# Performance work log

Measured on AMD Instinct MI355X. Metric: run time of the kernel, lower is better.

Reference implementation:

```python
import jax, jax.numpy as jnp
import numpy as np

B, S, H = 2, 2048, 2048
NH, HD = 16, 128


def rotate_half(x):
    x1, x2 = x[..., : x.shape[-1] // 2], x[..., x.shape[-1] // 2 :]
    return jnp.concatenate((-x2, x1), axis=-1)


def setup_inputs() -> dict:
    key = jax.random.key(0)
    ks = jax.random.split(key, 8)
    return {
        "hidden": jax.random.normal(ks[0], (B, S, H), dtype=jnp.float32),
        "cos": jax.random.uniform(ks[1], (S, HD), dtype=jnp.float32),
        "sin": jax.random.uniform(ks[2], (S, HD), dtype=jnp.float32),
        "attention_mask": jnp.zeros((B, 1, S, S), dtype=jnp.float32),
        "Wq": jax.random.normal(ks[3], (H, H), dtype=jnp.float32) * 0.02,
        "Wk": jax.random.normal(ks[4], (H, H), dtype=jnp.float32) * 0.02,
        "Wv": jax.random.normal(ks[5], (H, H), dtype=jnp.float32) * 0.02,
        "Wo": jax.random.normal(ks[6], (H, H), dtype=jnp.float32) * 0.02,
    }


def reference(hidden, cos, sin, attention_mask, Wq, Wk, Wv, Wo):
    b, s, h = hidden.shape
    # torch Linear: y = x @ W.T ; reshape to [B, NH, S, HD]
    def proj(W):
        return (hidden @ W.T).reshape(b, s, NH, HD).transpose(0, 2, 1, 3)

    q, k, v = proj(Wq), proj(Wk), proj(Wv)
    c = cos[None, None, :, :]  # [1,1,S,HD]
    si = sin[None, None, :, :]
    q = q * c + rotate_half(q) * si
    k = k * c + rotate_half(k) * si
    scores = jnp.einsum("bhqd,bhkd->bhqk", q, k) / jnp.sqrt(jnp.float32(HD))
    scores = scores + attention_mask
    attn = jax.nn.softmax(scores.astype(jnp.float32), axis=-1).astype(q.dtype)
    out = jnp.einsum("bhqk,bhkd->bhqd", attn, v)
    out = out.transpose(0, 2, 1, 3).reshape(b, s, h)
    return out @ Wo.T
```

## Files before the change

kernel.cpp:

```cpp
#include <hip/hip_runtime.h>
#include <hip/hip_bf16.h>
#include <math.h>

#define SEQ 2048
#define HID 2048
#define NHEAD 16
#define HDIM 128
#define LDK 4096

typedef __bf16 bf16_t;
typedef __bf16 bf16x2 __attribute__((ext_vector_type(2)));
typedef __bf16 bf16x4_t __attribute__((ext_vector_type(4)));
typedef __bf16 bf16x8 __attribute__((ext_vector_type(8)));
typedef float f32x4 __attribute__((ext_vector_type(4)));
typedef float f32x16 __attribute__((ext_vector_type(16)));
typedef unsigned u32x4 __attribute__((ext_vector_type(4)));

#define MFMA16(a, b, c) __builtin_amdgcn_mfma_f32_16x16x32_bf16(a, b, c, 0, 0, 0)
#define MFMA32(a, b, c) __builtin_amdgcn_mfma_f32_32x32x16_bf16(a, b, c, 0, 0, 0)
#define GLOAD_LDS(g, l) \
  __builtin_amdgcn_global_load_lds((const __attribute__((address_space(1))) void*)(g), \
                                   (__attribute__((address_space(3))) void*)(l), 16, 0, 0)

static __device__ inline unsigned pk2(float lo, float hi) {
  bf16x2 t; t[0] = (bf16_t)lo; t[1] = (bf16_t)hi;
  return __builtin_bit_cast(unsigned, t);
}

static __device__ inline bf16x8 pack_slice(const float* p, int hi) {
  unsigned A1 = pk2(p[0], p[1]);
  unsigned A2 = pk2(p[2], p[3]);
  unsigned B1 = pk2(p[4], p[5]);
  unsigned B2 = pk2(p[6], p[7]);
  unsigned A1s = __shfl_xor(A1, 32, 64);
  unsigned A2s = __shfl_xor(A2, 32, 64);
  unsigned B1s = __shfl_xor(B1, 32, 64);
  unsigned B2s = __shfl_xor(B2, 32, 64);
  unsigned w0 = hi ? B1s : A1;
  unsigned w1 = hi ? B2s : A2;
  unsigned w2 = hi ? B1 : A1s;
  unsigned w3 = hi ? B2 : A2s;
  u32x4 W = {w0, w1, w2, w3};
  return __builtin_bit_cast(bf16x8, W);
}

__global__ void cast_hidden(const float* __restrict__ in, bf16_t* __restrict__ out) {
  int i = blockIdx.x * 256 + threadIdx.x;
  float4 v = ((const float4*)in)[i];
  bf16x4_t b;
  b[0] = (bf16_t)v.x; b[1] = (bf16_t)v.y; b[2] = (bf16_t)v.z; b[3] = (bf16_t)v.w;
  ((bf16x4_t*)out)[i] = b;
}

__global__ void cast_weights(const float* __restrict__ a, const float* __restrict__ b,
                             const float* __restrict__ c, const float* __restrict__ d,
                             bf16_t* __restrict__ out) {
  const float* srcs[4] = {a, b, c, d};
  const float* src = srcs[blockIdx.y];
  bf16_t* dst = out + (size_t)blockIdx.y * (HID * HID);
  int i = blockIdx.x * 256 + threadIdx.x;
  float4 v = ((const float4*)src)[i];
  bf16x4_t o;
  o[0] = (bf16_t)v.x; o[1] = (bf16_t)v.y; o[2] = (bf16_t)v.z; o[3] = (bf16_t)v.w;
  ((bf16x4_t*)dst)[i] = o;
}

__global__ __launch_bounds__(512, 2) void gemm256(
    const bf16_t* __restrict__ A, const bf16_t* __restrict__ Bw,
    bf16_t* __restrict__ Cb, float* __restrict__ Cf, int M, int N, int K) {
  __shared__ char smem[131072];
  const int tid = threadIdx.x, lane = tid & 63, wid = tid >> 6;
  const int wr = wid >> 2, wc = wid & 3;
  const int lr = lane & 15, lg = lane >> 4;
  const int xcd = blockIdx.x & 7, l = blockIdx.x >> 3;
  const int brow = (xcd >> 2) * 8 + (l >> 2);
  const int bcol = (xcd & 3) * 4 + (l & 3);
  const int NT = K >> 6;

  const bf16_t* Ab = A + (size_t)(brow * 256) * K;
  const bf16_t* Bb = Bw + (size_t)(bcol * 256) * K;

  f32x4 acc[8][4] = {};
  bf16x8 af[4], bfr[4];
  const int swz = (lg ^ ((lr >> 1) & 3)) << 4;

#define STAGE_HALF(t_, op, kh)                                                        \
  {                                                                                   \
    int tt = (t_) < NT ? (t_) : NT - 1;                                               \
    const bf16_t* gsrc = (op) ? Bb : Ab;                                              \
    char* ldst = smem + (tt & 1) * 65536 + (op) * 32768 + (kh) * 16384;               \
    _Pragma("unroll") for (int is = 0; is < 2; ++is) {                                \
      int p = tid + is * 512;                                                         \
      int row = p >> 2, ch = p & 3;                                                   \
      GLOAD_LDS(gsrc + (size_t)row * K + tt * 64 + (kh) * 32 +                        \
                    ((ch ^ ((row >> 1) & 3)) * 8),                                    \
                ldst + p * 16);                                                       \
    }                                                                                 \
  }

#define PHASE(cb, kh, mh, LOADB, STAGECALL, VM)                                       \
  {                                                                                   \
    _Pragma("unroll") for (int mf = 0; mf < 4; ++mf) {                                \
      int row = wr * 128 + (mh) * 64 + mf * 16 + lr;                                  \
      af[mf] = *(const bf16x8*)(smem + (cb) * 65536 + (kh) * 16384 + row * 64 + swz); \
    }                                                                                 \
    if (LOADB) {                                                                      \
      _Pragma("unroll") for (int nf = 0; nf < 4; ++nf) {                              \
        int row = wc * 64 + nf * 16 + lr;                                             \
        bfr[nf] = *(const bf16x8*)(smem + (cb) * 65536 + 32768 + (kh) * 16384 +       \
                                   row * 64 + swz);                                   \
      }                                                                               \
    }                                                                                 \
    STAGECALL;                                                                        \
    __builtin_amdgcn_s_barrier();                                                     \
    asm volatile("s_waitcnt lgkmcnt(0)" ::: "memory");                                \
    __builtin_amdgcn_sched_barrier(0);                                                \
    __builtin_amdgcn_s_setprio(1);                                                    \
    _Pragma("unroll") for (int mf = 0; mf < 4; ++mf)                                  \
      _Pragma("unroll") for (int nf = 0; nf < 4; ++nf)                                \
        acc[(mh) * 4 + mf][nf] = MFMA16(af[mf], bfr[nf], acc[(mh) * 4 + mf][nf]);     \
    __builtin_amdgcn_s_setprio(0);                                                    \
    if (VM) { asm volatile("s_waitcnt vmcnt(6)" ::: "memory"); }                      \
    __builtin_amdgcn_s_barrier();                                                     \
    __builtin_amdgcn_sched_barrier(0);                                                \
  }

  STAGE_HALF(0, 1, 0); STAGE_HALF(0, 0, 0); STAGE_HALF(0, 1, 1); STAGE_HALF(0, 0, 1);
  STAGE_HALF(1, 1, 0); STAGE_HALF(1, 0, 0); STAGE_HALF(1, 1, 1);
  asm volatile("s_waitcnt vmcnt(6)" ::: "memory");
  __builtin_amdgcn_s_barrier();
  __builtin_amdgcn_sched_barrier(0);

  const int NI = NT >> 1;
  for (int i = 0; i < NI; ++i) {
    const int t2 = 2 * i;
    PHASE(0, 0, 0, 1, STAGE_HALF(t2 + 1, 0, 1), 0);
    PHASE(0, 0, 1, 0, STAGE_HALF(t2 + 2, 1, 0), 0);
    PHASE(0, 1, 0, 1, STAGE_HALF(t2 + 2, 0, 0), 0);
    PHASE(0, 1, 1, 0, STAGE_HALF(t2 + 2, 1, 1), 1);
    PHASE(1, 0, 0, 1, STAGE_HALF(t2 + 2, 0, 1), 0);
    PHASE(1, 0, 1, 0, STAGE_HALF(t2 + 3, 1, 0), 0);
    PHASE(1, 1, 0, 1, STAGE_HALF(t2 + 3, 0, 0), 0);
    PHASE(1, 1, 1, 0, STAGE_HALF(t2 + 3, 1, 1), 1);
  }
#undef PHASE
#undef STAGE_HALF

#pragma unroll
  for (int mi = 0; mi < 8; ++mi)
#pragma unroll
    for (int nf = 0; nf < 4; ++nf)
#pragma unroll
      for (int r = 0; r < 4; ++r) {
        int row = brow * 256 + wr * 128 + (mi >> 2) * 64 + (mi & 3) * 16 + lg * 4 + r;
        int col = bcol * 256 + wc * 64 + nf * 16 + lr;
        float v = acc[mi][nf][r];
        if (Cf) Cf[(size_t)row * N + col] = v;
        else    Cb[(size_t)row * N + col] = (bf16_t)v;
      }
}

__global__ __launch_bounds__(256, 3) void gemm_bt(
    const bf16_t* __restrict__ A, const bf16_t* __restrict__ Bw,
    bf16_t* __restrict__ Cb, float* __restrict__ Cf,
    int M, int N, int K) {
  __shared__ bf16_t As[2][128 * 32];
  __shared__ bf16_t Bs[2][128 * 32];
  const int tid = threadIdx.x;
  const int lane = tid & 63, wid = tid >> 6;
  const int wr = wid >> 1, wc = wid & 1;
  const int lr = lane & 15, lg = lane >> 4;
  const int nwg = gridDim.x;
  const int lid = (blockIdx.x & 7) * (nwg >> 3) + (blockIdx.x >> 3);
  const int nbc = N >> 7;
  const int brow = lid / nbc, bcol = lid % nbc;

  f32x4 acc[4][4] = {};
  const int swz = lg ^ ((lr >> 1) & 3);

  const int srow = tid >> 2, sch = tid & 3;
#define GSTAGE(k0, bb)                                                                   \
  {                                                                                      \
    _Pragma("unroll") for (int is = 0; is < 2; ++is) {                                   \
      int row = srow + is * 64;                                                          \
      int g = (sch ^ ((row >> 1) & 3)) * 8;                                              \
      GLOAD_LDS(A + (size_t)(brow * 128 + row) * K + (k0) + g,                           \
                &As[bb][(row * 4 + sch) * 8]);                                           \
      GLOAD_LDS(Bw + (size_t)(bcol * 128 + row) * K + (k0) + g,                          \
                &Bs[bb][(row * 4 + sch) * 8]);                                           \
    }                                                                                    \
  }

  GSTAGE(0, 0);
  __syncthreads();

  const int nt = K / 32;
  for (int t = 0; t < nt; ++t) {
    const int cb = t & 1;
    if (t + 1 < nt) GSTAGE((t + 1) * 32, cb ^ 1);
    bf16x8 af[4], bfr[4];
#pragma unroll
    for (int m = 0; m < 4; ++m)
      af[m] = *(const bf16x8*)(&As[cb][(wr * 64 + m * 16 + lr) * 32 + swz * 8]);
#pragma unroll
    for (int n = 0; n < 4; ++n)
      bfr[n] = *(const bf16x8*)(&Bs[cb][(wc * 64 + n * 16 + lr) * 32 + swz * 8]);
#pragma unroll
    for (int m = 0; m < 4; ++m)
#pragma unroll
      for (int n = 0; n < 4; ++n)
        acc[m][n] = MFMA16(af[m], bfr[n], acc[m][n]);
    __syncthreads();
  }
#undef GSTAGE

#pragma unroll
  for (int m = 0; m < 4; ++m)
#pragma unroll
    for (int n = 0; n < 4; ++n)
#pragma unroll
      for (int r = 0; r < 4; ++r) {
        int row = brow * 128 + wr * 64 + m * 16 + lg * 4 + r;
        int col = bcol * 128 + wc * 64 + n * 16 + lr;
        float v = acc[m][n][r];
        if (Cf) Cf[(size_t)row * N + col] = v;
        else    Cb[(size_t)row * N + col] = (bf16_t)v;
      }
}

__global__ void rope_qk(bf16_t* __restrict__ QK,
                        const float* __restrict__ cost, const float* __restrict__ sint) {
  const float SCALE = 0.08838834764831845f;
  int idx = blockIdx.x * 256 + threadIdx.x;
  int d8 = idx & 7;
  int t = idx >> 3;
  int h = t & 15;
  int row = t >> 4;
  int s = row & (SEQ - 1);
  size_t base = (size_t)row * LDK + h * HDIM;
  const float4* cp = (const float4*)(cost + s * HDIM);
  const float4* sp = (const float4*)(sint + s * HDIM);
  float4 c0a = cp[d8 * 2], c0b = cp[d8 * 2 + 1];
  float4 c1a = cp[16 + d8 * 2], c1b = cp[16 + d8 * 2 + 1];
  float4 s0a = sp[d8 * 2], s0b = sp[d8 * 2 + 1];
  float4 s1a = sp[16 + d8 * 2], s1b = sp[16 + d8 * 2 + 1];
  float c0[8] = {c0a.x, c0a.y, c0a.z, c0a.w, c0b.x, c0b.y, c0b.z, c0b.w};
  float c1[8] = {c1a.x, c1a.y, c1a.z, c1a.w, c1b.x, c1b.y, c1b.z, c1b.w};
  float s0[8] = {s0a.x, s0a.y, s0a.z, s0a.w, s0b.x, s0b.y, s0b.z, s0b.w};
  float s1[8] = {s1a.x, s1a.y, s1a.z, s1a.w, s1b.x, s1b.y, s1b.z, s1b.w};

  bf16_t* Q = QK;
  bf16_t* K = QK + 2048;
  bf16x8 qlo = *(bf16x8*)(Q + base + d8 * 8);
  bf16x8 qhi = *(bf16x8*)(Q + base + 64 + d8 * 8);
  bf16x8 klo = *(bf16x8*)(K + base + d8 * 8);
  bf16x8 khi = *(bf16x8*)(K + base + 64 + d8 * 8);
  bf16x8 qlo2, qhi2, klo2, khi2;
#pragma unroll
  for (int j = 0; j < 8; ++j) {
    float q0 = (float)qlo[j], q1 = (float)qhi[j];
    qlo2[j] = (bf16_t)((q0 * c0[j] - q1 * s0[j]) * SCALE);
    qhi2[j] = (bf16_t)((q1 * c1[j] + q0 * s1[j]) * SCALE);
    float k0 = (float)klo[j], k1 = (float)khi[j];
    klo2[j] = (bf16_t)(k0 * c0[j] - k1 * s0[j]);
    khi2[j] = (bf16_t)(k1 * c1[j] + k0 * s1[j]);
  }
  *(bf16x8*)(Q + base + d8 * 8) = qlo2;
  *(bf16x8*)(Q + base + 64 + d8 * 8) = qhi2;
  *(bf16x8*)(K + base + d8 * 8) = klo2;
  *(bf16x8*)(K + base + 64 + d8 * 8) = khi2;
}

__global__ void transpose_v(const bf16_t* __restrict__ Vf, bf16_t* __restrict__ Vt) {
  __shared__ bf16_t t[32][33];
  int tx = threadIdx.x & 31, ty = threadIdx.x >> 5;
  int r0 = blockIdx.y * 32, c0 = blockIdx.x * 32;
#pragma unroll
  for (int j = 0; j < 4; ++j)
    t[ty + j * 8][tx] = Vf[(size_t)(r0 + ty + j * 8) * HID + c0 + tx];
  __syncthreads();
#pragma unroll
  for (int j = 0; j < 4; ++j) {
    int c = c0 + ty + j * 8;
    int r = r0 + tx;
    int h = c >> 7, d = c & 127, b = r >> 11, s = r & (SEQ - 1);
    Vt[(((size_t)(b * NHEAD + h)) * HDIM + d) * SEQ + s] = t[tx][ty + j * 8];
  }
}

__global__ void mask_pack(const float* __restrict__ m, bf16_t* __restrict__ mp) {
  __shared__ float t[32][33];
  int tx = threadIdx.x & 31, ty = threadIdx.x >> 5;
  int q0 = blockIdx.x * 32, k0 = blockIdx.y * 32;
  const float* mb = m + (size_t)blockIdx.z * SEQ * SEQ;
#pragma unroll
  for (int j = 0; j < 4; ++j)
    t[ty + j * 8][tx] = mb[(size_t)(q0 + ty + j * 8) * SEQ + k0 + tx];
  __syncthreads();
  int r = tx & 15, hi = tx >> 4;
  int kl = (r & 3) + 8 * (r >> 2) + 4 * hi;
  bf16_t* ob = mp + ((size_t)(blockIdx.z * 64 + blockIdx.y) * 2048 + q0) * 32;
#pragma unroll
  for (int j = 0; j < 4; ++j) {
    int qloc = ty + j * 8;
    ob[(size_t)qloc * 32 + tx] = (bf16_t)t[qloc][kl];
  }
}

__global__ __launch_bounds__(512, 2) void flash_fwd(
    const bf16_t* __restrict__ Qf, const bf16_t* __restrict__ Kf,
    const bf16_t* __restrict__ Vt, const bf16_t* __restrict__ maskP,
    bf16_t* __restrict__ AO) {
  __shared__ char smem[131072];
  char* KsB = smem;
  char* VsB = smem + 65536;
  const int tid = threadIdx.x, lane = tid & 63, wid = tid >> 6;
  const int q32 = lane & 31, hi = lane >> 5;

  const int x = blockIdx.x;
  const int bh = x & 31, qt = x >> 5;
  const int b = bh >> 4, h = bh & 15;
  const int qg = qt * 256 + wid * 32 + q32;

  bf16x8 qf[8];
  const bf16_t* qptr = Qf + (size_t)(b * SEQ + qg) * LDK + h * HDIM + hi * 8;
#pragma unroll
  for (int ds = 0; ds < 8; ++ds) qf[ds] = *(const bf16x8*)(qptr + ds * 16);

  const bf16_t* mQ = maskP + (size_t)b * 64 * 65536 + (size_t)qg * 32 + hi * 16;

  float mrun = -INFINITY, lpart = 0.f;
  f32x16 o[4] = {};
  const int lswz = (q32 & 15) << 4;

#define STAGE_KV(kt_, bb)                                                                \
  {                                                                                      \
    const int kb0_ = (kt_) * 128;                                                        \
    _Pragma("unroll") for (int is = 0; is < 4; ++is) {                                   \
      int p = tid + is * 512;                                                            \
      int row = p >> 4, ch = p & 15;                                                     \
      int src = (ch * 16) ^ ((row & 15) << 4);                                           \
      GLOAD_LDS((const char*)(Kf + (size_t)(b * SEQ + kb0_ + row) * LDK + h * HDIM) +    \
                    src,                                                                 \
                KsB + (bb) * 32768 + p * 16);                                            \
      GLOAD_LDS((const char*)(Vt + (size_t)(bh * HDIM + row) * SEQ + kb0_) + src,        \
                VsB + (bb) * 32768 + p * 16);                                            \
    }                                                                                    \
  }

  STAGE_KV(0, 0);
  __syncthreads();

  const int NT = SEQ / 128;
  for (int kt = 0; kt < NT; ++kt) {
    const int cur = kt & 1;
    if (kt + 1 < NT) STAGE_KV(kt + 1, cur ^ 1);

    bf16x8 mk[8];
#pragma unroll
    for (int kb = 0; kb < 4; ++kb) {
      const size_t mo = (size_t)(kt * 4 + kb) * 65536;
      mk[2 * kb]     = *(const bf16x8*)(mQ + mo);
      mk[2 * kb + 1] = *(const bf16x8*)(mQ + mo + 8);
    }
    f32x16 sacc[4];
#pragma unroll
    for (int kb = 0; kb < 4; ++kb)
#pragma unroll
      for (int r = 0; r < 8; ++r) {
        sacc[kb][r]     = (float)mk[2 * kb][r];
        sacc[kb][8 + r] = (float)mk[2 * kb + 1][r];
      }

    const char* Kbase = KsB + cur * 32768 + q32 * 256;
#pragma unroll
    for (int ds = 0; ds < 8; ++ds) {
      const int co = (ds * 32 + hi * 16) ^ lswz;
#pragma unroll
      for (int kb = 0; kb < 4; ++kb) {
        bf16x8 kfr = *(const bf16x8*)(Kbase + kb * 8192 + co);
        sacc[kb] = MFMA32(kfr, qf[ds], sacc[kb]);
      }
    }

    f32x16 mm;
#pragma unroll
    for (int r = 0; r < 16; ++r)
      mm[r] = fmaxf(fmaxf(sacc[0][r], sacc[1][r]), fmaxf(sacc[2][r], sacc[3][r]));
    float e0 = fmaxf(fmaxf(mm[0], mm[1]), fmaxf(mm[2], mm[3]));
    float e1 = fmaxf(fmaxf(mm[4], mm[5]), fmaxf(mm[6], mm[7]));
    float e2 = fmaxf(fmaxf(mm[8], mm[9]), fmaxf(mm[10], mm[11]));
    float e3 = fmaxf(fmaxf(mm[12], mm[13]), fmaxf(mm[14], mm[15]));
    float mx = fmaxf(fmaxf(e0, e1), fmaxf(e2, e3));
    mx = fmaxf(mx, __shfl_xor(mx, 32, 64));
    if (!__all(mx <= mrun + 8.f)) {
      float mnew = fmaxf(mrun, mx);
      float corr = __expf(mrun - mnew);
      mrun = mnew; lpart *= corr;
#pragma unroll
      for (int d0 = 0; d0 < 4; ++d0)
#pragma unroll
        for (int r = 0; r < 16; ++r) o[d0][r] *= corr;
    }

#pragma unroll
    for (int kb = 0; kb < 4; ++kb) {
      float p_[16];
#pragma unroll
      for (int r = 0; r < 16; ++r) p_[r] = __expf(sacc[kb][r] - mrun);
      {
        float t0 = (p_[0] + p_[1]) + (p_[2] + p_[3]);
        float t1 = (p_[4] + p_[5]) + (p_[6] + p_[7]);
        float t2 = (p_[8] + p_[9]) + (p_[10] + p_[11]);
        float t3 = (p_[12] + p_[13]) + (p_[14] + p_[15]);
        lpart += (t0 + t1) + (t2 + t3);
      }
#pragma unroll
      for (int s = 0; s < 2; ++s) {
        bf16x8 pav = pack_slice(p_ + 8 * s, hi);
        const int gs = kb * 2 + s;
        const char* Vbase = VsB + cur * 32768 + q32 * 256;
#pragma unroll
        for (int d0 = 0; d0 < 4; ++d0) {
          bf16x8 vf = *(const bf16x8*)(Vbase + d0 * 8192 +
                                       ((gs * 32 + hi * 16) ^ lswz));
          o[d0] = MFMA32(vf, pav, o[d0]);
        }
      }
    }
    __syncthreads();
  }
#undef STAGE_KV

  float l = lpart + __shfl_xor(lpart, 32, 64);
  float rl = 1.f / l;
  bf16_t* aorow = AO + (size_t)(b * SEQ + qg) * HID + h * HDIM;
#pragma unroll
  for (int d0 = 0; d0 < 4; ++d0)
#pragma unroll
    for (int g = 0; g < 4; ++g) {
      unsigned lo = pk2(o[d0][4 * g + 0] * rl, o[d0][4 * g + 1] * rl);
      unsigned hi2 = pk2(o[d0][4 * g + 2] * rl, o[d0][4 * g + 3] * rl);
      int d = d0 * 32 + 8 * g + 4 * hi;
      *(unsigned*)(aorow + d) = lo;
      *(unsigned*)(aorow + d + 2) = hi2;
    }
}

extern "C" void kernel_launch(void* const* d_in, const int* in_sizes, int n_in,
                              void* d_out, int out_size, void* d_ws, size_t ws_size,
                              hipStream_t stream) {
  const float* hidden = (const float*)d_in[0];
  const float* cost   = (const float*)d_in[1];
  const float* sint   = (const float*)d_in[2];
  const float* mask   = (const float*)d_in[3];
  const float* Wq     = (const float*)d_in[4];
  const float* Wk     = (const float*)d_in[5];
  const float* Wv     = (const float*)d_in[6];
  const float* Wo     = (const float*)d_in[7];
  float* out = (float*)d_out;
  char* ws = (char*)d_ws;

  bf16_t* Af    = (bf16_t*)(ws + 0);
  bf16_t* Wqb   = (bf16_t*)(ws + 16777216);
  bf16_t* Wvb   = (bf16_t*)(ws + 33554432);
  bf16_t* Wob   = (bf16_t*)(ws + 41943040);
  bf16_t* QK    = (bf16_t*)(ws + 50331648);
  bf16_t* Vf    = (bf16_t*)(ws + 83886080);
  bf16_t* Vt    = (bf16_t*)(ws + 0);
  bf16_t* maskP = (bf16_t*)(ws + 83886080);
  bf16_t* AO    = (bf16_t*)(ws + 16777216);

  cast_hidden<<<8192, 256, 0, stream>>>(hidden, Af);
  cast_weights<<<dim3(4096, 4), 256, 0, stream>>>(Wq, Wk, Wv, Wo, Wqb);

  gemm256<<<256, 512, 0, stream>>>(Af, Wqb, QK, nullptr, 4096, LDK, HID);
  gemm_bt<<<512, 256, 0, stream>>>(Af, Wvb, Vf, nullptr, 4096, HID, HID);

  rope_qk<<<2048, 256, 0, stream>>>(QK, cost, sint);
  transpose_v<<<dim3(64, 128), 256, 0, stream>>>(Vf, Vt);
  mask_pack<<<dim3(64, 64, 2), 256, 0, stream>>>(mask, maskP);

  flash_fwd<<<256, 512, 0, stream>>>(QK, QK + 2048, Vt, maskP, AO);

  gemm_bt<<<512, 256, 0, stream>>>(AO, Wob, nullptr, out, 4096, HID, HID);
}
```

Baseline: 319.8 us.

## Pipeline QK MFMA chains with per-block softmax using exp2 and permlane swap

Restructures the flash attention inner loop so the QK^T chain for key block kb+1 is issued before the softmax and PV work for block kb, keeping a per-block online max instead of one max per 128-key tile. Folds log2(e) into the Q scale and the packed mask so the softmax can use raw v_exp_f32 (exp2) rather than __expf. Replaces four shuffles plus selects in P packing with v_permlane32_swap. Adds s_setprio around MFMA chains and raises the lazy-rescale threshold to suit base-2. Checking the max more often may trigger more rescales, and the interleaving adds register pressure.

```diff
diff --git a/kernel.cpp b/kernel.cpp
--- a/kernel.cpp
+++ b/kernel.cpp
@@ -27,20 +27,20 @@
   return __builtin_bit_cast(unsigned, t);
 }
 
-static __device__ inline bf16x8 pack_slice(const float* p, int hi) {
+static __device__ inline float exp2_fast(float x) {
+  float r;
+  asm("v_exp_f32 %0, %1" : "=v"(r) : "v"(x));
+  return r;
+}
+
+static __device__ inline bf16x8 pack_slice(const float* p) {
   unsigned A1 = pk2(p[0], p[1]);
   unsigned A2 = pk2(p[2], p[3]);
   unsigned B1 = pk2(p[4], p[5]);
   unsigned B2 = pk2(p[6], p[7]);
-  unsigned A1s = __shfl_xor(A1, 32, 64);
-  unsigned A2s = __shfl_xor(A2, 32, 64);
-  unsigned B1s = __shfl_xor(B1, 32, 64);
-  unsigned B2s = __shfl_xor(B2, 32, 64);
-  unsigned w0 = hi ? B1s : A1;
-  unsigned w1 = hi ? B2s : A2;
-  unsigned w2 = hi ? B1 : A1s;
-  unsigned w3 = hi ? B2 : A2s;
-  u32x4 W = {w0, w1, w2, w3};
+  asm("v_permlane32_swap_b32 %0, %1" : "+v"(A1), "+v"(B1));
+  asm("v_permlane32_swap_b32 %0, %1" : "+v"(A2), "+v"(B2));
+  u32x4 W = {A1, A2, B1, B2};
   return __builtin_bit_cast(bf16x8, W);
 }
 
@@ -230,7 +230,7 @@
 
 __global__ void rope_qk(bf16_t* __restrict__ QK,
                         const float* __restrict__ cost, const float* __restrict__ sint) {
-  const float SCALE = 0.08838834764831845f;
+  const float SCALE = 0.12751569978848444f;
   int idx = blockIdx.x * 256 + threadIdx.x;
   int d8 = idx & 7;
   int t = idx >> 3;
@@ -289,6 +289,7 @@
 }
 
 __global__ void mask_pack(const float* __restrict__ m, bf16_t* __restrict__ mp) {
+  const float L2E = 1.4426950408889634f;
   __shared__ float t[32][33];
   int tx = threadIdx.x & 31, ty = threadIdx.x >> 5;
   int q0 = blockIdx.x * 32, k0 = blockIdx.y * 32;
@@ -303,7 +304,7 @@
 #pragma unroll
   for (int j = 0; j < 4; ++j) {
     int qloc = ty + j * 8;
-    ob[(size_t)qloc * 32 + tx] = (bf16_t)t[qloc][kl];
+    ob[(size_t)qloc * 32 + tx] = (bf16_t)(t[qloc][kl] * L2E);
   }
 }
 
@@ -348,6 +349,24 @@
     }                                                                                    \
   }
 
+#define INIT_SACC(kb)                                                                    \
+  {                                                                                      \
+    _Pragma("unroll") for (int r = 0; r < 8; ++r) {                                      \
+      sacc[kb][r]     = (float)mk[2 * (kb)][r];                                          \
+      sacc[kb][8 + r] = (float)mk[2 * (kb) + 1][r];                                      \
+    }                                                                                    \
+  }
+#define QK_CHAIN(kb)                                                                     \
+  {                                                                                      \
+    const char* Kb_ = KsB + cur * 32768 + q32 * 256 + (kb) * 8192;                       \
+    __builtin_amdgcn_s_setprio(1);                                                       \
+    _Pragma("unroll") for (int ds = 0; ds < 8; ++ds) {                                   \
+      bf16x8 kfr = *(const bf16x8*)(Kb_ + ((ds * 32 + hi * 16) ^ lswz));                 \
+      sacc[kb] = MFMA32(kfr, qf[ds], sacc[kb]);                                          \
+    }                                                                                    \
+    __builtin_amdgcn_s_setprio(0);                                                       \
+  }
+
   STAGE_KV(0, 0);
   __syncthreads();
 
@@ -363,51 +382,38 @@
       mk[2 * kb]     = *(const bf16x8*)(mQ + mo);
       mk[2 * kb + 1] = *(const bf16x8*)(mQ + mo + 8);
     }
+
     f32x16 sacc[4];
-#pragma unroll
-    for (int kb = 0; kb < 4; ++kb)
-#pragma unroll
-      for (int r = 0; r < 8; ++r) {
-        sacc[kb][r]     = (float)mk[2 * kb][r];
-        sacc[kb][8 + r] = (float)mk[2 * kb + 1][r];
-      }
-
-    const char* Kbase = KsB + cur * 32768 + q32 * 256;
-#pragma unroll
-    for (int ds = 0; ds < 8; ++ds) {
-      const int co = (ds * 32 + hi * 16) ^ lswz;
-#pragma unroll
-      for (int kb = 0; kb < 4; ++kb) {
-        bf16x8 kfr = *(const bf16x8*)(Kbase + kb * 8192 + co);
-        sacc[kb] = MFMA32(kfr, qf[ds], sacc[kb]);
-      }
-    }
-
-    f32x16 mm;
-#pragma unroll
-    for (int r = 0; r < 16; ++r)
-      mm[r] = fmaxf(fmaxf(sacc[0][r], sacc[1][r]), fmaxf(sacc[2][r], sacc[3][r]));
-    float e0 = fmaxf(fmaxf(mm[0], mm[1]), fmaxf(mm[2], mm[3]));
-    float e1 = fmaxf(fmaxf(mm[4], mm[5]), fmaxf(mm[6], mm[7]));
-    float e2 = fmaxf(fmaxf(mm[8], mm[9]), fmaxf(mm[10], mm[11]));
-    float e3 = fmaxf(fmaxf(mm[12], mm[13]), fmaxf(mm[14], mm[15]));
-    float mx = fmaxf(fmaxf(e0, e1), fmaxf(e2, e3));
-    mx = fmaxf(mx, __shfl_xor(mx, 32, 64));
-    if (!__all(mx <= mrun + 8.f)) {
-      float mnew = fmaxf(mrun, mx);
-      float corr = __expf(mrun - mnew);
-      mrun = mnew; lpart *= corr;
-#pragma unroll
-      for (int d0 = 0; d0 < 4; ++d0)
-#pragma unroll
-        for (int r = 0; r < 16; ++r) o[d0][r] *= corr;
-    }
+    INIT_SACC(0);
+    QK_CHAIN(0);
 
 #pragma unroll
     for (int kb = 0; kb < 4; ++kb) {
+      if (kb < 3) {
+        INIT_SACC(kb + 1);
+        QK_CHAIN(kb + 1);
+      }
+
+      float a0 = fmaxf(fmaxf(sacc[kb][0], sacc[kb][1]), fmaxf(sacc[kb][2], sacc[kb][3]));
+      float a1 = fmaxf(fmaxf(sacc[kb][4], sacc[kb][5]), fmaxf(sacc[kb][6], sacc[kb][7]));
+      float a2 = fmaxf(fmaxf(sacc[kb][8], sacc[kb][9]), fmaxf(sacc[kb][10], sacc[kb][11]));
+      float a3 = fmaxf(fmaxf(sacc[kb][12], sacc[kb][13]),
+                       fmaxf(sacc[kb][14], sacc[kb][15]));
+      float mx = fmaxf(fmaxf(a0, a1), fmaxf(a2, a3));
+      mx = fmaxf(mx, __shfl_xor(mx, 32, 64));
+      if (!__all(mx <= mrun + 11.5f)) {
+        float mnew = fmaxf(mrun, mx);
+        float corr = exp2_fast(mrun - mnew);
+        mrun = mnew; lpart *= corr;
+#pragma unroll
+        for (int d0 = 0; d0 < 4; ++d0)
+#pragma unroll
+          for (int r = 0; r < 16; ++r) o[d0][r] *= corr;
+      }
+
       float p_[16];
 #pragma unroll
-      for (int r = 0; r < 16; ++r) p_[r] = __expf(sacc[kb][r] - mrun);
+      for (int r = 0; r < 16; ++r) p_[r] = exp2_fast(sacc[kb][r] - mrun);
       {
         float t0 = (p_[0] + p_[1]) + (p_[2] + p_[3]);
         float t1 = (p_[4] + p_[5]) + (p_[6] + p_[7]);
@@ -415,22 +421,27 @@
         float t3 = (p_[12] + p_[13]) + (p_[14] + p_[15]);
         lpart += (t0 + t1) + (t2 + t3);
       }
+
+      const char* Vbase = VsB + cur * 32768 + q32 * 256;
 #pragma unroll
       for (int s = 0; s < 2; ++s) {
-        bf16x8 pav = pack_slice(p_ + 8 * s, hi);
+        bf16x8 pav = pack_slice(p_ + 8 * s);
         const int gs = kb * 2 + s;
-        const char* Vbase = VsB + cur * 32768 + q32 * 256;
+        __builtin_amdgcn_s_setprio(1);
 #pragma unroll
         for (int d0 = 0; d0 < 4; ++d0) {
           bf16x8 vf = *(const bf16x8*)(Vbase + d0 * 8192 +
                                        ((gs * 32 + hi * 16) ^ lswz));
           o[d0] = MFMA32(vf, pav, o[d0]);
         }
+        __builtin_amdgcn_s_setprio(0);
       }
     }
     __syncthreads();
   }
 #undef STAGE_KV
+#undef INIT_SACC
+#undef QK_CHAIN
 
   float l = lpart + __shfl_xor(lpart, 32, 64);
   float rl = 1.f / l;
```

Result: faster. 312.4 us (-2.3%).
